# Performance work log

Measured on AMD Instinct MI355X. Metric: run time of the kernel, lower is better.

## Reference

```python
import jax, jax.numpy as jnp
import numpy as np
from jax import lax

T, D, H, TAGS = 2048, 1024, 2048, 1024

def setup_inputs() -> dict:
    key = jax.random.key(0)
    ks = jax.random.split(key, 7)
    s = 1.0 / np.sqrt(H)
    return {
        "x": jax.random.normal(ks[0], (T, D), dtype=jnp.float32),
        "W_ih": jax.random.normal(ks[1], (4 * H, D), dtype=jnp.float32) * s,
        "W_hh": jax.random.normal(ks[2], (4 * H, H), dtype=jnp.float32) * s,
        "b_ih": jax.random.normal(ks[3], (4 * H,), dtype=jnp.float32) * s,
        "b_hh": jax.random.normal(ks[4], (4 * H,), dtype=jnp.float32) * s,
        "W_out": jax.random.normal(ks[5], (TAGS, H), dtype=jnp.float32) * s,
        "b_out": jax.random.normal(ks[6], (TAGS,), dtype=jnp.float32) * s,
    }

def reference(x, W_ih, W_hh, b_ih, b_hh, W_out, b_out):
    Hd = W_hh.shape[1]
    # Precompute input-side gate pre-activations for all timesteps: [T, 4H]
    x_gates = x @ W_ih.T + (b_ih + b_hh)

    def step(carry, xg_t):
        h, c = carry  # [H], [H]
        g = xg_t + h @ W_hh.T  # [4H]
        i, f, gg, o = jnp.split(g, 4)  # PyTorch gate order: i, f, g, o
        i = jax.nn.sigmoid(i)
        f = jax.nn.sigmoid(f)
        gg = jnp.tanh(gg)
        o = jax.nn.sigmoid(o)
        c = f * c + i * gg
        h = o * jnp.tanh(c)
        return (h, c), h

    h0 = jnp.zeros((Hd,), dtype=x.dtype)
    c0 = jnp.zeros((Hd,), dtype=x.dtype)
    _, hs = lax.scan(step, (h0, c0), x_gates)  # hs: [T, H]

    tag_space = hs @ W_out.T + b_out  # [T, TAGS]
    return jax.nn.log_softmax(tag_space, axis=1)
```

## Files before the change

kernel.cpp:

```cpp
#include <hip/hip_runtime.h>
#include <hip/hip_bf16.h>

#define TT    2048
#define DD    1024
#define HH    2048
#define TAGS_ 1024
#define G4    8192

typedef float f32x4 __attribute__((ext_vector_type(4)));
typedef __bf16 bf16x8 __attribute__((ext_vector_type(8)));
typedef _Float16 f16x2 __attribute__((ext_vector_type(2)));
typedef _Float16 f16x4 __attribute__((ext_vector_type(4)));
typedef unsigned u32x2 __attribute__((ext_vector_type(2)));

__device__ __forceinline__ unsigned short f2bf(float f) {
    unsigned u = __float_as_uint(f);
    unsigned r = (u + 0x7fffu + ((u >> 16) & 1u)) >> 16;
    return (unsigned short)r;
}

__device__ __forceinline__ f16x2 u2h(unsigned u) {
    return __builtin_bit_cast(f16x2, u);
}

#if __has_builtin(__builtin_amdgcn_fdot2)
#define FDOT2(a, b, c) __builtin_amdgcn_fdot2((a), (b), (c), false)
#else
__device__ __forceinline__ float FDOT2(f16x2 a, f16x2 b, float c) {
    return fmaf((float)a.x, (float)b.x, fmaf((float)a.y, (float)b.y, c));
}
#endif

__global__ __launch_bounds__(256) void cvt_bf16_k(const float* __restrict__ in,
                                                  unsigned short* __restrict__ out, int n) {
    int i = (blockIdx.x * 256 + threadIdx.x) * 4;
    if (i < n) {
        float4 v = *(const float4*)(in + i);
        ushort4 o;
        o.x = f2bf(v.x); o.y = f2bf(v.y); o.z = f2bf(v.z); o.w = f2bf(v.w);
        *(ushort4*)(out + i) = o;
    }
}

__global__ __launch_bounds__(256) void cvt_f16_k(const float* __restrict__ in,
                                                 _Float16* __restrict__ out, int n) {
    int i = (blockIdx.x * 256 + threadIdx.x) * 4;
    if (i < n) {
        float4 v = *(const float4*)(in + i);
        f16x4 o;
        o.x = (_Float16)v.x; o.y = (_Float16)v.y;
        o.z = (_Float16)v.z; o.w = (_Float16)v.w;
        *(f16x4*)(out + i) = o;
    }
}

__global__ __launch_bounds__(256) void cvt_lo16f_k(const unsigned* __restrict__ in,
                                                   unsigned short* __restrict__ out, int n) {
    int i = (blockIdx.x * 256 + threadIdx.x) * 4;
    if (i < n) {
        uint4 v = *(const uint4*)(in + i);
        ushort4 o;
        o.x = f2bf((float)__builtin_bit_cast(_Float16, (unsigned short)(v.x & 0xffff)));
        o.y = f2bf((float)__builtin_bit_cast(_Float16, (unsigned short)(v.y & 0xffff)));
        o.z = f2bf((float)__builtin_bit_cast(_Float16, (unsigned short)(v.z & 0xffff)));
        o.w = f2bf((float)__builtin_bit_cast(_Float16, (unsigned short)(v.w & 0xffff)));
        *(ushort4*)(out + i) = o;
    }
}

__global__ __launch_bounds__(256) void gemm_bt_k(const unsigned short* __restrict__ A,
                                                 const unsigned short* __restrict__ B,
                                                 void* __restrict__ Cv,
                                                 const float* __restrict__ bias1,
                                                 const float* __restrict__ bias2,
                                                 int M, int N, int K, int out_f16) {
    const int bn = blockIdx.x, bm = blockIdx.y;
    const int tid = threadIdx.x;
    const int wave = tid >> 6, lane = tid & 63;
    const int wm = (wave >> 1) * 64, wn = (wave & 1) * 64;

    __shared__ unsigned short As[128 * 64];
    __shared__ unsigned short Bs[128 * 64];

    f32x4 acc[4][4] = {};

    for (int k0 = 0; k0 < K; k0 += 64) {
#pragma unroll
        for (int i = 0; i < 4; ++i) {
            int bo = (tid + i * 256) * 16;
            int r = bo >> 7;
            int cb = bo & 127;
            *(uint4*)((char*)As + bo) =
                *(const uint4*)((const char*)(A + (size_t)(bm * 128 + r) * K + k0) + cb);
            *(uint4*)((char*)Bs + bo) =
                *(const uint4*)((const char*)(B + (size_t)(bn * 128 + r) * K + k0) + cb);
        }
        __syncthreads();
#pragma unroll
        for (int kk = 0; kk < 64; kk += 32) {
            int kb = kk + (lane >> 4) * 8;
            bf16x8 af[4], bfr[4];
#pragma unroll
            for (int mi = 0; mi < 4; ++mi)
                af[mi] = *(const bf16x8*)&As[(wm + mi * 16 + (lane & 15)) * 64 + kb];
#pragma unroll
            for (int ni = 0; ni < 4; ++ni)
                bfr[ni] = *(const bf16x8*)&Bs[(wn + ni * 16 + (lane & 15)) * 64 + kb];
#pragma unroll
            for (int mi = 0; mi < 4; ++mi)
#pragma unroll
                for (int ni = 0; ni < 4; ++ni)
                    acc[mi][ni] = __builtin_amdgcn_mfma_f32_16x16x32_bf16(
                        af[mi], bfr[ni], acc[mi][ni], 0, 0, 0);
        }
        __syncthreads();
    }

#pragma unroll
    for (int ni = 0; ni < 4; ++ni) {
        int col = bn * 128 + wn + ni * 16 + (lane & 15);
        float bv = bias1 ? bias1[col] : 0.0f;
        if (bias2) bv += bias2[col];
#pragma unroll
        for (int mi = 0; mi < 4; ++mi) {
            int row = bm * 128 + wm + mi * 16 + (lane >> 4) * 4;
#pragma unroll
            for (int r = 0; r < 4; ++r) {
                float v = acc[mi][ni][r] + bv;
                if (out_f16)
                    ((_Float16*)Cv)[(size_t)(row + r) * N + col] = (_Float16)v;
                else
                    ((float*)Cv)[(size_t)(row + r) * N + col] = v;
            }
        }
    }
}

__global__ __launch_bounds__(512, 2) void lstm_rec_k(const _Float16* __restrict__ Whh16,
                                                     const _Float16* __restrict__ xg,
                                                     unsigned* __restrict__ hs32) {
    const int tid = threadIdx.x;
    const int wave = tid >> 6;
    const int lane = tid & 63;
    const int unit = (blockIdx.x << 3) + wave;

    __shared__ unsigned hpk[2][1024];

    unsigned W[4][8][2];
#pragma unroll
    for (int g = 0; g < 4; ++g) {
        const _Float16* wr = Whh16 + ((size_t)(g * HH) + unit) * HH + (lane << 2);
#pragma unroll
        for (int k = 0; k < 8; ++k) {
            u32x2 v = *(const u32x2*)(wr + (k << 8));
            W[g][k][0] = v.x; W[g][k][1] = v.y;
        }
    }
#pragma unroll
    for (int g = 0; g < 4; ++g)
#pragma unroll
        for (int k = 0; k < 8; ++k)
            asm volatile("" : "+a"(W[g][k][0]), "+a"(W[g][k][1]));

    float creg = 0.0f;

    float xg0 = 0.f, xg1 = 0.f, xg2 = 0.f, xg3 = 0.f;
    if (lane == 0) {
        const _Float16* xr = xg + unit;
        xg0 = (float)xr[0]; xg1 = (float)xr[2048];
        xg2 = (float)xr[4096]; xg3 = (float)xr[6144];
    }

    for (int t = 0; t < TT; ++t) {
        const int buf = t & 1;

        float nx0 = 0.f, nx1 = 0.f, nx2 = 0.f, nx3 = 0.f;
        if (lane == 0 && t + 1 < TT) {
            const _Float16* xr = xg + ((size_t)(t + 1) << 13) + unit;
            nx0 = (float)xr[0]; nx1 = (float)xr[2048];
            nx2 = (float)xr[4096]; nx3 = (float)xr[6144];
        }

        const unsigned* pp = hs32 + ((size_t)t << 11) + (wave << 8) + (lane << 2);
        uint4 hv;
        const unsigned tu = (unsigned)t;
        for (;;) {
            asm volatile(
                "global_load_dwordx4 %0, %1, off sc0 sc1\n\t"
                "s_waitcnt vmcnt(0)"
                : "=&v"(hv) : "v"(pp));
            int ok = (hv.x >> 16) == tu && (hv.y >> 16) == tu &&
                     (hv.z >> 16) == tu && (hv.w >> 16) == tu;
            if (__all(ok)) break;
            __builtin_amdgcn_s_sleep(1);
        }

        unsigned plo = (hv.x & 0xffffu) | (hv.y << 16);
        unsigned phi = (hv.z & 0xffffu) | (hv.w << 16);
        u32x2 pk; pk.x = plo; pk.y = phi;
        *(u32x2*)&hpk[buf][(wave << 7) + (lane << 1)] = pk;
        __syncthreads();

        float acc0 = 0.f, acc1 = 0.f, acc2 = 0.f, acc3 = 0.f;
#define DOTK(kk) do {                                                          \
        u32x2 hp = *(const u32x2*)&hpk[buf][((kk) << 7) + (lane << 1)];        \
        f16x2 hlo = u2h(hp.x), hhi = u2h(hp.y);                                \
        acc0 = FDOT2(u2h(W[0][kk][0]), hlo, acc0);                             \
        acc0 = FDOT2(u2h(W[0][kk][1]), hhi, acc0);                             \
        acc1 = FDOT2(u2h(W[1][kk][0]), hlo, acc1);                             \
        acc1 = FDOT2(u2h(W[1][kk][1]), hhi, acc1);                             \
        acc2 = FDOT2(u2h(W[2][kk][0]), hlo, acc2);                             \
        acc2 = FDOT2(u2h(W[2][kk][1]), hhi, acc2);                             \
        acc3 = FDOT2(u2h(W[3][kk][0]), hlo, acc3);                             \
        acc3 = FDOT2(u2h(W[3][kk][1]), hhi, acc3);                             \
    } while (0)
        DOTK(0); DOTK(1); DOTK(2); DOTK(3);
        DOTK(4); DOTK(5); DOTK(6); DOTK(7);
#undef DOTK

#pragma unroll
        for (int off = 32; off >= 1; off >>= 1) {
            acc0 += __shfl_xor(acc0, off, 64);
            acc1 += __shfl_xor(acc1, off, 64);
            acc2 += __shfl_xor(acc2, off, 64);
            acc3 += __shfl_xor(acc3, off, 64);
        }

        if (lane == 0) {
            float gi = acc0 + xg0;
            float gf = acc1 + xg1;
            float gg = acc2 + xg2;
            float go = acc3 + xg3;
            float ei = __expf(-gi), ef = __expf(-gf), eo = __expf(-go);
            float eg = __expf(-2.0f * gg);
            float si = 1.0f / (1.0f + ei);
            float sf = 1.0f / (1.0f + ef);
            float so = 1.0f / (1.0f + eo);
            float tg = 2.0f / (1.0f + eg) - 1.0f;
            creg = sf * creg + si * tg;
            float ec = __expf(-2.0f * creg);
            float th = 2.0f / (1.0f + ec) - 1.0f;
            float h = so * th;
            _Float16 fh = (_Float16)h;
            unsigned word = ((unsigned)(t + 1) << 16) |
                            (unsigned)__builtin_bit_cast(unsigned short, fh);
            unsigned* hd = hs32 + (((size_t)(t + 1)) << 11) + unit;
            asm volatile("global_store_dword %0, %1, off sc0 sc1"
                         :: "v"(hd), "v"(word));
        }
        xg0 = nx0; xg1 = nx1; xg2 = nx2; xg3 = nx3;
    }
}

__global__ __launch_bounds__(256) void lsm_k(const float* __restrict__ tag,
                                             float* __restrict__ out) {
    const int row = blockIdx.x, tid = threadIdx.x;
    const int wave = tid >> 6, lane = tid & 63;
    const float* p = tag + ((size_t)row << 10);
    float v0 = p[tid], v1 = p[tid + 256], v2 = p[tid + 512], v3 = p[tid + 768];
    float m = fmaxf(fmaxf(v0, v1), fmaxf(v2, v3));
#pragma unroll
    for (int off = 32; off >= 1; off >>= 1) m = fmaxf(m, __shfl_xor(m, off, 64));
    __shared__ float redm[4];
    __shared__ float reds[4];
    if (lane == 0) redm[wave] = m;
    __syncthreads();
    m = fmaxf(fmaxf(redm[0], redm[1]), fmaxf(redm[2], redm[3]));
    float s = __expf(v0 - m) + __expf(v1 - m) + __expf(v2 - m) + __expf(v3 - m);
#pragma unroll
    for (int off = 32; off >= 1; off >>= 1) s += __shfl_xor(s, off, 64);
    if (lane == 0) reds[wave] = s;
    __syncthreads();
    s = reds[0] + reds[1] + reds[2] + reds[3];
    float lse = m + __logf(s);
    float* o = out + ((size_t)row << 10);
    o[tid] = v0 - lse; o[tid + 256] = v1 - lse;
    o[tid + 512] = v2 - lse; o[tid + 768] = v3 - lse;
}

extern "C" void kernel_launch(void* const* d_in, const int* in_sizes, int n_in,
                              void* d_out, int out_size, void* d_ws, size_t ws_size,
                              hipStream_t stream) {
    const float* x    = (const float*)d_in[0];
    const float* Wih  = (const float*)d_in[1];
    const float* Whh  = (const float*)d_in[2];
    const float* bih  = (const float*)d_in[3];
    const float* bhh  = (const float*)d_in[4];
    const float* Wout = (const float*)d_in[5];
    const float* bout = (const float*)d_in[6];
    float* out = (float*)d_out;

    char* ws = (char*)d_ws;
    size_t off = 0;
    unsigned* hs32 = (unsigned*)(ws + off); off += (size_t)(TT + 1) * HH * 4;
    float* tag = (float*)hs32;
    _Float16* xg = (_Float16*)(ws + off); off += (size_t)TT * G4 * 2;
    char* C = ws + off; off += (size_t)G4 * HH * 2;
    unsigned short* xbf    = (unsigned short*)(C);
    unsigned short* wihbf  = (unsigned short*)(C + ((size_t)TT * DD * 2) * 2);
    _Float16* Whh16        = (_Float16*)(C);
    unsigned short* woutbf = (unsigned short*)(C);
    unsigned short* hs     = (unsigned short*)(C + (size_t)4 * 1024 * 1024);

    hipMemsetAsync(hs32, 0, (size_t)(TT + 1) * HH * 4, stream);

    cvt_bf16_k<<<(TT * DD) / 1024, 256, 0, stream>>>(x, xbf, TT * DD);
    cvt_bf16_k<<<(G4 * DD) / 1024, 256, 0, stream>>>(Wih, wihbf, G4 * DD);

    gemm_bt_k<<<dim3(G4 / 128, TT / 128), 256, 0, stream>>>(xbf, wihbf, (void*)xg,
                                                            bih, bhh, TT, G4, DD, 1);

    cvt_f16_k<<<(G4 * HH) / 1024, 256, 0, stream>>>(Whh, Whh16, G4 * HH);

    {
        const _Float16* whh_p = Whh16;
        const _Float16* xg_p = xg;
        unsigned* hs32_p = hs32;
        void* args[] = {(void*)&whh_p, (void*)&xg_p, (void*)&hs32_p};
        hipLaunchCooperativeKernel((const void*)lstm_rec_k, dim3(256), dim3(512), args, 0,
                                   stream);
    }

    cvt_bf16_k<<<(TAGS_ * HH) / 1024, 256, 0, stream>>>(Wout, woutbf, TAGS_ * HH);
    cvt_lo16f_k<<<(TT * HH) / 1024, 256, 0, stream>>>(hs32 + HH, hs, TT * HH);

    gemm_bt_k<<<dim3(TAGS_ / 128, TT / 128), 256, 0, stream>>>(hs, woutbf, (void*)tag,
                                                               bout, nullptr,
                                                               TT, TAGS_, HH, 0);

    lsm_k<<<TT, 256, 0, stream>>>(tag, out);
}
```

Measured before the change: 5.468 ms.

## Pipeline flag polling, use DPP reductions and scalar x-gate loads in LSTM recurrence

The recurrence kernel's spin-wait changes from one blocking dwordx4 poll per iteration to three rotating batches of coalesced per-lane dword loads kept in flight. A new batch is reissued whenever a check fails, instead of sleeping. The cross-lane gate reduction uses a DPP row-shift/broadcast sum plus readlane in place of shfl_xor butterflies. Input-gate values are fetched each step with scalar loads that overlap the poll, and all lanes compute the activations uniformly. The aim is to shorten the per-timestep critical path of the serial recurrence, at the cost of more memory traffic during polling and extra register pressure.

```diff
diff --git a/kernel.cpp b/kernel.cpp
--- a/kernel.cpp
+++ b/kernel.cpp
@@ -30,6 +30,23 @@
     return fmaf((float)a.x, (float)b.x, fmaf((float)a.y, (float)b.y, c));
 }
 #endif
+
+__device__ __forceinline__ float dpp_sum64(float x) {
+    int t;
+    t = __builtin_amdgcn_update_dpp(0, __float_as_int(x), 0x111, 0xf, 0xf, true);
+    x += __int_as_float(t);
+    t = __builtin_amdgcn_update_dpp(0, __float_as_int(x), 0x112, 0xf, 0xf, true);
+    x += __int_as_float(t);
+    t = __builtin_amdgcn_update_dpp(0, __float_as_int(x), 0x114, 0xf, 0xf, true);
+    x += __int_as_float(t);
+    t = __builtin_amdgcn_update_dpp(0, __float_as_int(x), 0x118, 0xf, 0xf, true);
+    x += __int_as_float(t);
+    t = __builtin_amdgcn_update_dpp(0, __float_as_int(x), 0x142, 0xa, 0xf, true);
+    x += __int_as_float(t);
+    t = __builtin_amdgcn_update_dpp(0, __float_as_int(x), 0x143, 0xc, 0xf, true);
+    x += __int_as_float(t);
+    return __int_as_float(__builtin_amdgcn_readlane(__float_as_int(x), 63));
+}
 
 __global__ __launch_bounds__(256) void cvt_bf16_k(const float* __restrict__ in,
                                                   unsigned short* __restrict__ out, int n) {
@@ -144,7 +161,7 @@
     const int lane = tid & 63;
     const int unit = (blockIdx.x << 3) + wave;
 
-    __shared__ unsigned hpk[2][1024];
+    __shared__ unsigned short hbuf16[2][2048];
 
     unsigned W[4][8][2];
 #pragma unroll
@@ -164,92 +181,124 @@
 
     float creg = 0.0f;
 
-    float xg0 = 0.f, xg1 = 0.f, xg2 = 0.f, xg3 = 0.f;
-    if (lane == 0) {
-        const _Float16* xr = xg + unit;
-        xg0 = (float)xr[0]; xg1 = (float)xr[2048];
-        xg2 = (float)xr[4096]; xg3 = (float)xr[6144];
-    }
+    const unsigned sh = (unit & 1) << 4;
+    unsigned long long xbase = (unsigned long long)(uintptr_t)xg + ((unsigned)(unit << 1) & ~3u);
+
+#define ISSUE4(x0, x1, x2, x3)                                                \
+    asm volatile(                                                             \
+        "global_load_dword %0, %4, off sc0 sc1\n\t"                           \
+        "global_load_dword %1, %4, off offset:256 sc0 sc1\n\t"                \
+        "global_load_dword %2, %4, off offset:512 sc0 sc1\n\t"                \
+        "global_load_dword %3, %4, off offset:768 sc0 sc1"                    \
+        : "=&v"(x0), "=&v"(x1), "=&v"(x2), "=&v"(x3) : "v"(pp))
+#define WAIT8(x0, x1, x2, x3)                                                 \
+    asm volatile("s_waitcnt vmcnt(8)"                                         \
+                 : "+v"(x0), "+v"(x1), "+v"(x2), "+v"(x3) :: "memory")
+#define CHECK4(x0, x1, x2, x3)                                                \
+    __all((int)(((x0 >> 16) == tu) & ((x1 >> 16) == tu) &                     \
+                ((x2 >> 16) == tu) & ((x3 >> 16) == tu)))
 
     for (int t = 0; t < TT; ++t) {
         const int buf = t & 1;
-
-        float nx0 = 0.f, nx1 = 0.f, nx2 = 0.f, nx3 = 0.f;
-        if (lane == 0 && t + 1 < TT) {
-            const _Float16* xr = xg + ((size_t)(t + 1) << 13) + unit;
-            nx0 = (float)xr[0]; nx1 = (float)xr[2048];
-            nx2 = (float)xr[4096]; nx3 = (float)xr[6144];
-        }
-
-        const unsigned* pp = hs32 + ((size_t)t << 11) + (wave << 8) + (lane << 2);
-        uint4 hv;
         const unsigned tu = (unsigned)t;
+        const unsigned* pp = hs32 + ((size_t)t << 11) + (wave << 8) + lane;
+
+        unsigned a0, a1, a2, a3, b0, b1, b2, b3, c0, c1, c2, c3;
+        ISSUE4(a0, a1, a2, a3);
+        ISSUE4(b0, b1, b2, b3);
+        ISSUE4(c0, c1, c2, c3);
+
+        unsigned sd0, sd1, sd2, sd3;
+        {
+            unsigned long long xaddr = xbase + ((unsigned long long)t << 14);
+            unsigned alo = __builtin_amdgcn_readfirstlane((unsigned)xaddr);
+            unsigned ahi = __builtin_amdgcn_readfirstlane((unsigned)(xaddr >> 32));
+            unsigned long long ua = ((unsigned long long)ahi << 32) | alo;
+            asm volatile(
+                "s_load_dword %0, %4, 0x0\n\t"
+                "s_load_dword %1, %4, 0x1000\n\t"
+                "s_load_dword %2, %4, 0x2000\n\t"
+                "s_load_dword %3, %4, 0x3000\n\t"
+                "s_waitcnt lgkmcnt(0)"
+                : "=s"(sd0), "=s"(sd1), "=s"(sd2), "=s"(sd3)
+                : "s"(ua));
+        }
+        float xv0 = (float)__builtin_bit_cast(_Float16, (unsigned short)((sd0 >> sh) & 0xffffu));
+        float xv1 = (float)__builtin_bit_cast(_Float16, (unsigned short)((sd1 >> sh) & 0xffffu));
+        float xv2 = (float)__builtin_bit_cast(_Float16, (unsigned short)((sd2 >> sh) & 0xffffu));
+        float xv3 = (float)__builtin_bit_cast(_Float16, (unsigned short)((sd3 >> sh) & 0xffffu));
+
+        unsigned h0, h1, h2, h3;
         for (;;) {
-            asm volatile(
-                "global_load_dwordx4 %0, %1, off sc0 sc1\n\t"
-                "s_waitcnt vmcnt(0)"
-                : "=&v"(hv) : "v"(pp));
-            int ok = (hv.x >> 16) == tu && (hv.y >> 16) == tu &&
-                     (hv.z >> 16) == tu && (hv.w >> 16) == tu;
-            if (__all(ok)) break;
-            __builtin_amdgcn_s_sleep(1);
-        }
-
-        unsigned plo = (hv.x & 0xffffu) | (hv.y << 16);
-        unsigned phi = (hv.z & 0xffffu) | (hv.w << 16);
-        u32x2 pk; pk.x = plo; pk.y = phi;
-        *(u32x2*)&hpk[buf][(wave << 7) + (lane << 1)] = pk;
+            WAIT8(a0, a1, a2, a3);
+            if (CHECK4(a0, a1, a2, a3)) { h0 = a0; h1 = a1; h2 = a2; h3 = a3; break; }
+            ISSUE4(a0, a1, a2, a3);
+            WAIT8(b0, b1, b2, b3);
+            if (CHECK4(b0, b1, b2, b3)) { h0 = b0; h1 = b1; h2 = b2; h3 = b3; break; }
+            ISSUE4(b0, b1, b2, b3);
+            WAIT8(c0, c1, c2, c3);
+            if (CHECK4(c0, c1, c2, c3)) { h0 = c0; h1 = c1; h2 = c2; h3 = c3; break; }
+            ISSUE4(c0, c1, c2, c3);
+        }
+        asm volatile("s_waitcnt vmcnt(0)"
+                     : "+v"(a0), "+v"(a1), "+v"(a2), "+v"(a3),
+                       "+v"(b0), "+v"(b1), "+v"(b2), "+v"(b3),
+                       "+v"(c0), "+v"(c1), "+v"(c2), "+v"(c3) :: "memory");
+
+        {
+            unsigned short* hb = &hbuf16[buf][(wave << 8) + lane];
+            hb[0]   = (unsigned short)h0;
+            hb[64]  = (unsigned short)h1;
+            hb[128] = (unsigned short)h2;
+            hb[192] = (unsigned short)h3;
+        }
         __syncthreads();
 
-        float acc0 = 0.f, acc1 = 0.f, acc2 = 0.f, acc3 = 0.f;
-#define DOTK(kk) do {                                                          \
-        u32x2 hp = *(const u32x2*)&hpk[buf][((kk) << 7) + (lane << 1)];        \
-        f16x2 hlo = u2h(hp.x), hhi = u2h(hp.y);                                \
-        acc0 = FDOT2(u2h(W[0][kk][0]), hlo, acc0);                             \
-        acc0 = FDOT2(u2h(W[0][kk][1]), hhi, acc0);                             \
-        acc1 = FDOT2(u2h(W[1][kk][0]), hlo, acc1);                             \
-        acc1 = FDOT2(u2h(W[1][kk][1]), hhi, acc1);                             \
-        acc2 = FDOT2(u2h(W[2][kk][0]), hlo, acc2);                             \
-        acc2 = FDOT2(u2h(W[2][kk][1]), hhi, acc2);                             \
-        acc3 = FDOT2(u2h(W[3][kk][0]), hlo, acc3);                             \
-        acc3 = FDOT2(u2h(W[3][kk][1]), hhi, acc3);                             \
+        float g0 = 0.f, g1 = 0.f, g2 = 0.f, g3 = 0.f;
+#define DOTK(kk) do {                                                         \
+        u32x2 hp = *(const u32x2*)&hbuf16[buf][((kk) << 8) + (lane << 2)];    \
+        f16x2 hlo = u2h(hp.x), hhi = u2h(hp.y);                               \
+        g0 = FDOT2(u2h(W[0][kk][0]), hlo, g0);                                \
+        g0 = FDOT2(u2h(W[0][kk][1]), hhi, g0);                                \
+        g1 = FDOT2(u2h(W[1][kk][0]), hlo, g1);                                \
+        g1 = FDOT2(u2h(W[1][kk][1]), hhi, g1);                                \
+        g2 = FDOT2(u2h(W[2][kk][0]), hlo, g2);                                \
+        g2 = FDOT2(u2h(W[2][kk][1]), hhi, g2);                                \
+        g3 = FDOT2(u2h(W[3][kk][0]), hlo, g3);                                \
+        g3 = FDOT2(u2h(W[3][kk][1]), hhi, g3);                                \
     } while (0)
         DOTK(0); DOTK(1); DOTK(2); DOTK(3);
         DOTK(4); DOTK(5); DOTK(6); DOTK(7);
 #undef DOTK
 
-#pragma unroll
-        for (int off = 32; off >= 1; off >>= 1) {
-            acc0 += __shfl_xor(acc0, off, 64);
-            acc1 += __shfl_xor(acc1, off, 64);
-            acc2 += __shfl_xor(acc2, off, 64);
-            acc3 += __shfl_xor(acc3, off, 64);
-        }
+        float gi = dpp_sum64(g0) + xv0;
+        float gf = dpp_sum64(g1) + xv1;
+        float gg = dpp_sum64(g2) + xv2;
+        float go = dpp_sum64(g3) + xv3;
+
+        float ei = __expf(-gi), ef = __expf(-gf), eo = __expf(-go);
+        float eg = __expf(-2.0f * gg);
+        float si = 1.0f / (1.0f + ei);
+        float sf = 1.0f / (1.0f + ef);
+        float so = 1.0f / (1.0f + eo);
+        float tg = 2.0f / (1.0f + eg) - 1.0f;
+        creg = sf * creg + si * tg;
+        float ec = __expf(-2.0f * creg);
+        float th = 2.0f / (1.0f + ec) - 1.0f;
+        float h = so * th;
+        _Float16 fh = (_Float16)h;
+        unsigned word = ((tu + 1u) << 16) |
+                        (unsigned)__builtin_bit_cast(unsigned short, fh);
 
         if (lane == 0) {
-            float gi = acc0 + xg0;
-            float gf = acc1 + xg1;
-            float gg = acc2 + xg2;
-            float go = acc3 + xg3;
-            float ei = __expf(-gi), ef = __expf(-gf), eo = __expf(-go);
-            float eg = __expf(-2.0f * gg);
-            float si = 1.0f / (1.0f + ei);
-            float sf = 1.0f / (1.0f + ef);
-            float so = 1.0f / (1.0f + eo);
-            float tg = 2.0f / (1.0f + eg) - 1.0f;
-            creg = sf * creg + si * tg;
-            float ec = __expf(-2.0f * creg);
-            float th = 2.0f / (1.0f + ec) - 1.0f;
-            float h = so * th;
-            _Float16 fh = (_Float16)h;
-            unsigned word = ((unsigned)(t + 1) << 16) |
-                            (unsigned)__builtin_bit_cast(unsigned short, fh);
             unsigned* hd = hs32 + (((size_t)(t + 1)) << 11) + unit;
             asm volatile("global_store_dword %0, %1, off sc0 sc1"
                          :: "v"(hd), "v"(word));
         }
-        xg0 = nx0; xg1 = nx1; xg2 = nx2; xg3 = nx3;
-    }
+    }
+#undef ISSUE4
+#undef WAIT8
+#undef CHECK4
 }
 
 __global__ __launch_bounds__(256) void lsm_k(const float* __restrict__ tag,
```

New measurement: 10.33 ms. 89.0% more time.
